# Optimization experiments

Hardware: AMD Instinct MI355X
Metric: run time of the kernel (lower is better)

Reference implementation:

```python
import jax, jax.numpy as jnp
import numpy as np

B, S, E, H, C = 2, 2048, 1024, 16, 16
SQ2 = np.float32(np.sqrt(2.0))


def setup_inputs() -> dict:
    key = jax.random.key(0)
    ks = jax.random.split(key, 32)
    sc = 0.02
    d = {"query": jax.random.normal(ks[0], (B, S, E), jnp.float32)}
    i = 1
    for dom in ("f", "w", "c"):
        d[f"Wp_{dom}"] = jax.random.normal(ks[i], (E, E), jnp.float32) * sc; i += 1
        d[f"bp_{dom}"] = jnp.zeros((E,), jnp.float32)
        d[f"Wc_{dom}"] = jax.random.normal(ks[i], (C, E, 3), jnp.float32) * sc; i += 1
        d[f"bc_{dom}"] = jnp.zeros((C,), jnp.float32)
        d["F" + dom] = jax.random.normal(ks[i], (C, E), jnp.float32); i += 1
    d["mha_iw"] = jax.random.normal(ks[i], (3 * E, E), jnp.float32) * sc; i += 1
    d["mha_ib"] = jnp.zeros((3 * E,), jnp.float32)
    d["mha_ow"] = jax.random.normal(ks[i], (E, E), jnp.float32) * sc; i += 1
    d["mha_ob"] = jnp.zeros((E,), jnp.float32)
    d["fus_W"] = jax.random.normal(ks[i], (E, 3 * E), jnp.float32) * sc; i += 1
    d["fus_b"] = jnp.zeros((E,), jnp.float32)
    return d


def _conv1d(x, W, b):
    # x: [B,S,E] real -> [B,S,C], conv over sequence, kernel 3, same padding
    y = jax.lax.conv_general_dilated(x.transpose(0, 2, 1), W, (1,), [(1, 1)],
                                     dimension_numbers=("NCH", "OIH", "NCH"))
    return (y + b[None, :, None]).transpose(0, 2, 1)


def _channels(x, Wc, bc, Fp):
    # spectral conv (real/imag separately if complex) + adaptive softmax filtering
    if jnp.iscomplexobj(x):
        ch = _conv1d(x.real, Wc, bc) + 1j * _conv1d(x.imag, Wc, bc)
    else:
        ch = _conv1d(x, Wc, bc)
    fw = jax.nn.softmax(Fp, axis=0)  # [C,E], softmax over channels
    return jnp.einsum("bsc,ce->bse", ch, fw.astype(ch.dtype))


def _spec_attn(q, k, v):
    scale = np.float32(1.0) / jnp.sqrt(jnp.asarray(q.shape[-1], jnp.float32))
    scores = jnp.einsum("bse,bte->bst", q, k) * scale
    if jnp.iscomplexobj(scores):
        w = jax.nn.softmax(scores.real, axis=-1)
        cw = (w * jnp.exp(1j * jnp.angle(scores))).astype(jnp.complex64)
        return jnp.einsum("bst,bte->bse", cw, v)
    return jnp.einsum("bst,bte->bse", jax.nn.softmax(scores, axis=-1), v)


def _haar(x):
    # simplified Haar wavelet transform; S is a power of 2 so no padding needed
    cur, coeffs = x, []
    while cur.shape[1] > 1:
        e, o = cur[:, 0::2, :], cur[:, 1::2, :]
        coeffs.append((e - o) / SQ2)
        cur = (e + o) / SQ2
    coeffs.append(cur)
    return jnp.concatenate(coeffs[::-1], axis=1)


def _dct_mats(L):
    n = jnp.arange(L, dtype=jnp.float32)
    k = n[:, None]
    D = jnp.cos(np.pi * k * (2.0 * n + 1.0) / (2.0 * L))
    D = D.at[0].multiply(np.float32(np.sqrt(1.0 / L)))
    D = D.at[1:].multiply(np.float32(np.sqrt(2.0 / L)))
    I = jnp.cos(np.pi * n * (2.0 * k + 1.0) / (2.0 * L))
    I = I.at[:, 0].multiply(np.float32(np.sqrt(1.0 / L)))
    I = I.at[:, 1:].multiply(np.float32(np.sqrt(2.0 / L)))
    return D, I


def _domain(x, Wp, bp, Wc, bc, Fp, domain):
    # key=value=query so q_domain == k_domain == v_domain
    xd = x @ Wp.T + bp
    if domain == "fourier":
        s = jnp.fft.fft(xd, axis=1)
        ch = _channels(s, Wc, bc, Fp)
        out = _spec_attn(ch, ch, ch)
        return jnp.fft.ifft(out, axis=1).real
    elif domain == "wavelet":
        s = _haar(xd)
        ch = _channels(s, Wc, bc, Fp)
        return _spec_attn(ch, ch, ch)  # inverse wavelet is identity in source
    else:  # cosine
        D, I = _dct_mats(xd.shape[1])
        s = jnp.einsum("st,bte->bse", D, xd)
        ch = _channels(s, Wc, bc, Fp)
        out = _spec_attn(ch, ch, ch)
        return jnp.einsum("st,bte->bse", I, out)


def _mha(x, iw, ib, ow, ob, nheads):
    # torch nn.MultiheadAttention (batch_first) self-attention
    Bx, L, Ex = x.shape
    hd = Ex // nheads
    qkv = x @ iw.T + ib
    q, k, v = jnp.split(qkv, 3, axis=-1)
    sh = lambda t: t.reshape(Bx, L, nheads, hd).transpose(0, 2, 1, 3)
    q, k, v = sh(q), sh(k), sh(v)
    a = jax.nn.softmax(jnp.einsum("bhld,bhmd->bhlm", q, k) / np.float32(np.sqrt(hd)), axis=-1)
    o = jnp.einsum("bhlm,bhmd->bhld", a, v).transpose(0, 2, 1, 3).reshape(Bx, L, Ex)
    return o @ ow.T + ob


def reference(query, Wp_f, bp_f, Wc_f, bc_f, Ff, Wp_w, bp_w, Wc_w, bc_w, Fw,
              Wp_c, bp_c, Wc_c, bc_c, Fc, mha_iw, mha_ib, mha_ow, mha_ob, fus_W, fus_b):
    outs = [
        _domain(query, Wp_f, bp_f, Wc_f, bc_f, Ff, "fourier"),
        _domain(query, Wp_w, bp_w, Wc_w, bc_w, Fw, "wavelet"),
        _domain(query, Wp_c, bp_c, Wc_c, bc_c, Fc, "cosine"),
    ]
    Bq, Sq, Eq = query.shape
    stacked = jnp.stack(outs, axis=2)                 # [B,S,3,E]
    corr = _mha(stacked.reshape(Bq * Sq, 3, Eq), mha_iw, mha_ib, mha_ow, mha_ob, H)
    fused = corr.reshape(Bq, Sq, 3 * Eq)              # concat of correlated domain outputs
    return fused @ fus_W.T + fus_b
```

## Files before the change

kernel.cpp:

```cpp
#include <hip/hip_runtime.h>
#include <cmath>

#define BB 2
#define SS_ 2048
#define EE 1024
#define CC 16

typedef __attribute__((ext_vector_type(8))) short short8v;
typedef __attribute__((ext_vector_type(4))) float floatx4;

__device__ __forceinline__ void split4(const float4 v, short4& h, short4& l)
{
    unsigned ux = __float_as_uint(v.x), uy = __float_as_uint(v.y);
    unsigned uz = __float_as_uint(v.z), uw = __float_as_uint(v.w);
    h.x = (short)(ux >> 16); h.y = (short)(uy >> 16);
    h.z = (short)(uz >> 16); h.w = (short)(uw >> 16);
    float lx = v.x - __uint_as_float(ux & 0xFFFF0000u);
    float ly = v.y - __uint_as_float(uy & 0xFFFF0000u);
    float lz = v.z - __uint_as_float(uz & 0xFFFF0000u);
    float lw = v.w - __uint_as_float(uw & 0xFFFF0000u);
    l.x = (short)(__float_as_uint(lx) >> 16);
    l.y = (short)(__float_as_uint(ly) >> 16);
    l.z = (short)(__float_as_uint(lz) >> 16);
    l.w = (short)(__float_as_uint(lw) >> 16);
}

__device__ __forceinline__ void split1(float v, short& h, short& l)
{
    unsigned u = __float_as_uint(v);
    h = (short)(u >> 16);
    float rm = v - __uint_as_float(u & 0xFFFF0000u);
    l = (short)(__float_as_uint(rm) >> 16);
}

__device__ __forceinline__ void split4s(float a, float b, float c, float d,
                                        short4& h, short4& l)
{
    split1(a, h.x, l.x); split1(b, h.y, l.y);
    split1(c, h.z, l.z); split1(d, h.w, l.w);
}

__device__ __forceinline__ void split3_1(float v, short& x1, short& x2, short& x3)
{
    unsigned u = __float_as_uint(v);
    x1 = (short)(u >> 16);
    float r1 = v - __uint_as_float(u & 0xFFFF0000u);
    unsigned u2 = __float_as_uint(r1);
    x2 = (short)(u2 >> 16);
    float r2 = r1 - __uint_as_float(u2 & 0xFFFF0000u);
    x3 = (short)(__float_as_uint(r2) >> 16);
}

__device__ __forceinline__ void split3s(float a, float b, float c, float d,
                                        short4& h1, short4& h2, short4& h3)
{
    split3_1(a, h1.x, h2.x, h3.x); split3_1(b, h1.y, h2.y, h3.y);
    split3_1(c, h1.z, h2.z, h3.z); split3_1(d, h1.w, h2.w, h3.w);
}

__device__ __forceinline__ short4 neg4(short4 a)
{
    short4 r;
    r.x = (short)(a.x ^ (short)0x8000); r.y = (short)(a.y ^ (short)0x8000);
    r.z = (short)(a.z ^ (short)0x8000); r.w = (short)(a.w ^ (short)0x8000);
    return r;
}

__device__ __forceinline__ short8v pack8(short4 a, short4 b)
{
    short8v r;
    r[0] = a.x; r[1] = a.y; r[2] = a.z; r[3] = a.w;
    r[4] = b.x; r[5] = b.y; r[6] = b.z; r[7] = b.w;
    return r;
}

__device__ __forceinline__ short8v negbf(short8v x)
{
    int4 t = *(int4*)&x;
    t.x ^= 0x80008000; t.y ^= 0x80008000;
    t.z ^= 0x80008000; t.w ^= 0x80008000;
    return *(short8v*)&t;
}

#define BM 128
#define BN 128
#define BK 32
#define LDP 40

__launch_bounds__(256, 2)
__global__ void gemm_at(const float* __restrict__ A, const float* __restrict__ Bsrc,
                        float* __restrict__ C,
                        int K, int lda, int ldb, int ldc,
                        long sA, long sB, long sC, float alpha, int KS)
{
    __shared__ short sAh[BM * LDP], sAl[BM * LDP], sBh[BN * LDP], sBl[BN * LDP];
    const int z = blockIdx.z;
    const int bz = z / KS, ks = z % KS;
    const int klen = K / KS, kbase = ks * klen;
    A += (size_t)bz * sA; Bsrc += (size_t)bz * sB; C += (size_t)bz * sC;
    const int tid = threadIdx.x;
    const int m0 = blockIdx.y * BM, n0 = blockIdx.x * BN;

    const int lr0 = tid >> 3;
    const int kc0 = (tid & 7) * 4;
    const float* pa = A + (size_t)(m0 + lr0) * lda + kbase + kc0;
    const float* pb = Bsrc + (size_t)(n0 + lr0) * ldb + kbase + kc0;

    float4 ra[4], rb[4];
    #pragma unroll
    for (int c = 0; c < 4; ++c) {
        ra[c] = *(const float4*)(pa + (size_t)c * 32 * lda);
        rb[c] = *(const float4*)(pb + (size_t)c * 32 * ldb);
    }

    const int lane = tid & 63, wid = tid >> 6;
    const int wm = wid >> 1, wn = wid & 1;
    const int lr = lane & 15, qd = lane >> 4;
    const int arow = wm * 64 + lr;
    const int brow = wn * 64 + lr;
    const int koff = qd * 8;

    floatx4 acc[4][4];
    #pragma unroll
    for (int i = 0; i < 4; ++i)
        #pragma unroll
        for (int j = 0; j < 4; ++j)
            acc[i][j] = (floatx4){0.f, 0.f, 0.f, 0.f};

    for (int kt = 0; kt < klen; kt += BK) {
        __syncthreads();
        #pragma unroll
        for (int c = 0; c < 4; ++c) {
            const int row = lr0 + c * 32;
            short4 h, l;
            split4(ra[c], h, l);
            *(short4*)&sAh[row * LDP + kc0] = h;
            *(short4*)&sAl[row * LDP + kc0] = l;
            split4(rb[c], h, l);
            *(short4*)&sBh[row * LDP + kc0] = h;
            *(short4*)&sBl[row * LDP + kc0] = l;
        }
        __syncthreads();
        if (kt + BK < klen) {
            pa += BK; pb += BK;
            #pragma unroll
            for (int c = 0; c < 4; ++c) {
                ra[c] = *(const float4*)(pa + (size_t)c * 32 * lda);
                rb[c] = *(const float4*)(pb + (size_t)c * 32 * ldb);
            }
        }
        short8v ah[4], al[4], bh[4], bl[4];
        #pragma unroll
        for (int i = 0; i < 4; ++i) {
            ah[i] = *(const short8v*)&sAh[(arow + i * 16) * LDP + koff];
            al[i] = *(const short8v*)&sAl[(arow + i * 16) * LDP + koff];
            bh[i] = *(const short8v*)&sBh[(brow + i * 16) * LDP + koff];
            bl[i] = *(const short8v*)&sBl[(brow + i * 16) * LDP + koff];
        }
        #pragma unroll
        for (int i = 0; i < 4; ++i)
            #pragma unroll
            for (int j = 0; j < 4; ++j)
                acc[i][j] = __builtin_amdgcn_mfma_f32_16x16x32_bf16(ah[i], bh[j], acc[i][j], 0, 0, 0);
        #pragma unroll
        for (int i = 0; i < 4; ++i)
            #pragma unroll
            for (int j = 0; j < 4; ++j)
                acc[i][j] = __builtin_amdgcn_mfma_f32_16x16x32_bf16(ah[i], bl[j], acc[i][j], 0, 0, 0);
        #pragma unroll
        for (int i = 0; i < 4; ++i)
            #pragma unroll
            for (int j = 0; j < 4; ++j)
                acc[i][j] = __builtin_amdgcn_mfma_f32_16x16x32_bf16(al[i], bh[j], acc[i][j], 0, 0, 0);
    }

    #pragma unroll
    for (int i = 0; i < 4; ++i) {
        const int mbase = m0 + wm * 64 + i * 16 + qd * 4;
        #pragma unroll
        for (int j = 0; j < 4; ++j) {
            const int n = n0 + wn * 64 + j * 16 + lr;
            #pragma unroll
            for (int r = 0; r < 4; ++r)
                atomicAdd(&C[(size_t)(mbase + r) * ldc + n], alpha * acc[i][j][r]);
        }
    }
}

template<int NT, int MODE>
__launch_bounds__(256, 4)
__global__ void skmfma(const float* __restrict__ A0, const float* __restrict__ A1,
                       const float* __restrict__ B0, const float* __restrict__ B1,
                       float* __restrict__ C0, float* __restrict__ C1,
                       int K, int lda, int ldb, int ldc,
                       long sA, long sB, long sC, float alpha, int KS)
{
    constexpr int NA = (MODE >= 1) ? 2 : 1;
    constexpr int NB = (MODE == 2) ? 2 : 1;
    constexpr int NACC = (MODE == 1) ? 2 : 1;
    constexpr int CT = NT / 16;
    __shared__ short sAh[NA][64 * 40], sAl[NA][64 * 40];
    __shared__ short sBh[NB][NT * 40], sBl[NB][NT * 40];
    const int z = blockIdx.z;
    const int zb = z / KS, ks = z % KS;
    const int klen = K / KS, kbase = ks * klen;
    const float* Ap[NA]; const float* Bp[NB]; float* Cp[NACC];
    Ap[0] = A0 + (size_t)zb * sA;
    if constexpr (NA == 2) Ap[1] = A1 + (size_t)zb * sA;
    Bp[0] = B0 + (size_t)zb * sB;
    if constexpr (NB == 2) Bp[1] = B1 + (size_t)zb * sB;
    Cp[0] = C0 + (size_t)zb * sC;
    if constexpr (NACC == 2) Cp[1] = C1 + (size_t)zb * sC;

    const int tid = threadIdx.x;
    const int m0 = blockIdx.x * 64;
    const int arow = tid >> 2, akc = (tid & 3) * 8;
    const int lane = tid & 63, w = tid >> 6;
    const int lr = lane & 15, qd = lane >> 4;

    floatx4 acc[NACC][CT];
    #pragma unroll
    for (int s = 0; s < NACC; ++s)
        #pragma unroll
        for (int j = 0; j < CT; ++j)
            acc[s][j] = (floatx4){0.f, 0.f, 0.f, 0.f};

    for (int kc = 0; kc < klen; kc += 32) {
        __syncthreads();
        #pragma unroll
        for (int s = 0; s < NA; ++s) {
            const float* pa = Ap[s] + (size_t)(m0 + arow) * lda + kbase + kc + akc;
            float4 v0 = *(const float4*)pa;
            float4 v1 = *(const float4*)(pa + 4);
            short4 h, l;
            split4(v0, h, l);
            *(short4*)&sAh[s][arow * 40 + akc] = h;
            *(short4*)&sAl[s][arow * 40 + akc] = l;
            split4(v1, h, l);
            *(short4*)&sAh[s][arow * 40 + akc + 4] = h;
            *(short4*)&sAl[s][arow * 40 + akc + 4] = l;
        }
        #pragma unroll
        for (int s = 0; s < NB; ++s) {
            for (int lin = tid; lin < 32 * (NT / 4); lin += 256) {
                int kk = lin / (NT / 4), n4 = (lin % (NT / 4)) * 4;
                float4 v = *(const float4*)(Bp[s] + (size_t)(kbase + kc + kk) * ldb + n4);
                short4 h, l; split4(v, h, l);
                sBh[s][(n4 + 0) * 40 + kk] = h.x; sBh[s][(n4 + 1) * 40 + kk] = h.y;
                sBh[s][(n4 + 2) * 40 + kk] = h.z; sBh[s][(n4 + 3) * 40 + kk] = h.w;
                sBl[s][(n4 + 0) * 40 + kk] = l.x; sBl[s][(n4 + 1) * 40 + kk] = l.y;
                sBl[s][(n4 + 2) * 40 + kk] = l.z; sBl[s][(n4 + 3) * 40 + kk] = l.w;
            }
        }
        __syncthreads();
        short8v ah[NA], alv[NA];
        #pragma unroll
        for (int s = 0; s < NA; ++s) {
            ah[s]  = *(const short8v*)&sAh[s][(w * 16 + lr) * 40 + qd * 8];
            alv[s] = *(const short8v*)&sAl[s][(w * 16 + lr) * 40 + qd * 8];
        }
        short8v bh[NB][CT], bl[NB][CT];
        #pragma unroll
        for (int s = 0; s < NB; ++s)
            #pragma unroll
            for (int j = 0; j < CT; ++j) {
                bh[s][j] = *(const short8v*)&sBh[s][(j * 16 + lr) * 40 + qd * 8];
                bl[s][j] = *(const short8v*)&sBl[s][(j * 16 + lr) * 40 + qd * 8];
            }
        if constexpr (MODE == 0) {
            #pragma unroll
            for (int j = 0; j < CT; ++j) {
                acc[0][j] = __builtin_amdgcn_mfma_f32_16x16x32_bf16(ah[0], bh[0][j], acc[0][j], 0, 0, 0);
                acc[0][j] = __builtin_amdgcn_mfma_f32_16x16x32_bf16(ah[0], bl[0][j], acc[0][j], 0, 0, 0);
                acc[0][j] = __builtin_amdgcn_mfma_f32_16x16x32_bf16(alv[0], bh[0][j], acc[0][j], 0, 0, 0);
            }
        } else if constexpr (MODE == 1) {
            #pragma unroll
            for (int j = 0; j < CT; ++j) {
                acc[0][j] = __builtin_amdgcn_mfma_f32_16x16x32_bf16(ah[0], bh[0][j], acc[0][j], 0, 0, 0);
                acc[0][j] = __builtin_amdgcn_mfma_f32_16x16x32_bf16(ah[0], bl[0][j], acc[0][j], 0, 0, 0);
                acc[0][j] = __builtin_amdgcn_mfma_f32_16x16x32_bf16(alv[0], bh[0][j], acc[0][j], 0, 0, 0);
                acc[1][j] = __builtin_amdgcn_mfma_f32_16x16x32_bf16(ah[1], bh[0][j], acc[1][j], 0, 0, 0);
                acc[1][j] = __builtin_amdgcn_mfma_f32_16x16x32_bf16(ah[1], bl[0][j], acc[1][j], 0, 0, 0);
                acc[1][j] = __builtin_amdgcn_mfma_f32_16x16x32_bf16(alv[1], bh[0][j], acc[1][j], 0, 0, 0);
            }
        } else {
            #pragma unroll
            for (int j = 0; j < CT; ++j) {
                acc[0][j] = __builtin_amdgcn_mfma_f32_16x16x32_bf16(ah[0], bh[0][j], acc[0][j], 0, 0, 0);
                acc[0][j] = __builtin_amdgcn_mfma_f32_16x16x32_bf16(ah[0], bl[0][j], acc[0][j], 0, 0, 0);
                acc[0][j] = __builtin_amdgcn_mfma_f32_16x16x32_bf16(alv[0], bh[0][j], acc[0][j], 0, 0, 0);
                acc[0][j] = __builtin_amdgcn_mfma_f32_16x16x32_bf16(ah[1], bh[1][j], acc[0][j], 0, 0, 0);
                acc[0][j] = __builtin_amdgcn_mfma_f32_16x16x32_bf16(ah[1], bl[1][j], acc[0][j], 0, 0, 0);
                acc[0][j] = __builtin_amdgcn_mfma_f32_16x16x32_bf16(alv[1], bh[1][j], acc[0][j], 0, 0, 0);
            }
        }
    }
    #pragma unroll
    for (int s = 0; s < NACC; ++s)
        #pragma unroll
        for (int j = 0; j < CT; ++j) {
            const int n = j * 16 + lr;
            const int mb = m0 + w * 16 + qd * 4;
            #pragma unroll
            for (int r = 0; r < 4; ++r)
                atomicAdd(&Cp[s][(size_t)(mb + r) * ldc + n], alpha * acc[s][j][r]);
        }
}

__global__ void gen_trig(float* __restrict__ Cc, float* __restrict__ Sn,
                         float* __restrict__ D, float* __restrict__ I)
{
    size_t idx = (size_t)blockIdx.x * 256 + threadIdx.x;
    if (idx < 4194304) {
        int k = (int)(idx >> 11);
        int n = (int)(idx & 2047);
        int m = (k * n) & 2047;
        float ang = (float)(6.283185307179586 * (double)m / 2048.0);
        Cc[idx] = cosf(ang);
        Sn[idx] = -sinf(ang);
    } else {
        idx -= 4194304;
        int i = (int)(idx >> 11);
        int j = (int)(idx & 2047);
        const float r1 = 0.022097086912079608f;
        const float r2 = 0.03125f;
        const float pif = 3.14159265358979323846f;
        float a  = (pif * (float)i) * (float)(2 * j + 1) / 4096.0f;
        D[idx] = cosf(a) * (i == 0 ? r1 : r2);
        float ai = (pif * (float)j) * (float)(2 * i + 1) / 4096.0f;
        I[idx] = cosf(ai) * (j == 0 ? r1 : r2);
    }
}

__launch_bounds__(256)
__global__ void prep_fw_G(const float* __restrict__ F0, const float* __restrict__ F1,
                          const float* __restrict__ F2, float* __restrict__ fwT,
                          float* __restrict__ G)
{
    const int d = blockIdx.x, tid = threadIdx.x;
    const float* Fp = d == 0 ? F0 : (d == 1 ? F1 : F2);
    __shared__ float sf[CC * 1028];
    #pragma unroll
    for (int k = 0; k < 4; ++k) {
        int e = tid + k * 256;
        float v[CC]; float m = -3.4e38f;
        #pragma unroll
        for (int c = 0; c < CC; ++c) { v[c] = Fp[c * EE + e]; m = fmaxf(m, v[c]); }
        float s = 0.f;
        #pragma unroll
        for (int c = 0; c < CC; ++c) { v[c] = expf(v[c] - m); s += v[c]; }
        float inv = 1.f / s;
        #pragma unroll
        for (int c = 0; c < CC; ++c) { v[c] *= inv; sf[c * 1028 + e] = v[c]; }
        #pragma unroll
        for (int j = 0; j < 4; ++j)
            *(float4*)(fwT + d * 16384 + (size_t)e * 16 + j * 4) = *(float4*)&v[j * 4];
    }
    __syncthreads();
    const int a = tid >> 4, b = tid & 15;
    const float4* pa = (const float4*)&sf[a * 1028];
    const float4* pb = (const float4*)&sf[b * 1028];
    float s = 0.f;
    for (int i = 0; i < 256; ++i) {
        float4 x = pa[i], y = pb[i];
        s += x.x * y.x + x.y * y.y + x.z * y.z + x.w * y.w;
    }
    G[d * 256 + a * 16 + b] = s * 0.03125f;
}

__global__ void build_w2(const float* __restrict__ W0, const float* __restrict__ W1,
                         const float* __restrict__ W2_, float* __restrict__ W2cat)
{
    int idx = blockIdx.x * 256 + threadIdx.x;
    if (idx >= 3 * CC * EE * 3) return;
    int d = idx / 49152, r = idx % 49152;
    const float* Wc = d == 0 ? W0 : (d == 1 ? W1 : W2_);
    int c = r / 3072, e = (r % 3072) / 3, k = r % 3;
    W2cat[d * 49152 + e * 48 + c * 3 + k] = Wc[r];
}

__global__ void build_ub2(const float* __restrict__ b0, const float* __restrict__ b1,
                          const float* __restrict__ b2, const float* __restrict__ W2cat,
                          float* __restrict__ ub)
{
    const int d = blockIdx.x, tid = threadIdx.x;
    const float* bp = d == 0 ? b0 : (d == 1 ? b1 : b2);
    __shared__ float red[4][48];
    const int c = tid & 63, sl = tid >> 6;
    float s = 0.f;
    if (c < 48)
        for (int e = sl; e < EE; e += 4)
            s += bp[e] * W2cat[d * 49152 + e * 48 + c];
    if (c < 48) red[sl][c] = s;
    __syncthreads();
    if (tid < 48) ub[d * 48 + tid] = red[0][tid] + red[1][tid] + red[2][tid] + red[3][tid];
}

__launch_bounds__(256)
__global__ void build_yb2(const float* __restrict__ ob, const float* __restrict__ fus_W,
                          const float* __restrict__ fus_b, float* __restrict__ yb)
{
    const int n = blockIdx.x * 4 + (threadIdx.x >> 6);
    const int lane = threadIdx.x & 63;
    float s = 0.f;
    for (int j = lane; j < 3072; j += 64)
        s += ob[j & 1023] * fus_W[(size_t)n * 3072 + j];
    #pragma unroll
    for (int off = 32; off > 0; off >>= 1) s += __shfl_xor(s, off, 64);
    if (lane == 0) yb[n] = s + fus_b[n];
}

__global__ void init_all(float* __restrict__ zone1, const float* __restrict__ ub,
                         float* __restrict__ Pt, float* __restrict__ FTb,
                         float* __restrict__ out, const float* __restrict__ yb)
{
    size_t idx = (size_t)blockIdx.x * 256 + threadIdx.x;
    const size_t W3N = 147456, UN = 589824, ZN = 720896;
    const size_t Z1 = W3N + UN + ZN;
    const size_t PTN = 156672, FTN = 3145728, ON = 4194304;
    if (idx < Z1) {
        float v = 0.f;
        if (idx >= W3N && idx < W3N + UN) {
            size_t r = idx - W3N;
            int d = (int)(r / 196608), c = (int)(r % 48);
            v = ub[d * 48 + c];
        }
        zone1[idx] = v;
    } else if (idx < Z1 + PTN) {
        Pt[idx - Z1] = 0.f;
    } else if (idx < Z1 + PTN + FTN) {
        FTb[idx - Z1 - PTN] = 0.f;
    } else if (idx < Z1 + PTN + FTN + ON) {
        size_t r = idx - Z1 - PTN - FTN;
        out[r] = yb[r & 1023];
    }
}

__global__ void ib_append(const float* __restrict__ ib, float* __restrict__ Pt)
{
    int idx = blockIdx.x * 256 + threadIdx.x;
    if (idx >= 9216) return;
    int d = idx / 3072, j = idx % 3072;
    Pt[d * 52224 + j * 17 + 16] = ib[j];
}

__launch_bounds__(256)
__global__ void build_M(const float* __restrict__ Pt, float* __restrict__ Mten)
{
    int blk = blockIdx.x;
    int h = blk / 9, lm = blk % 9;
    int l = lm / 3, m = lm % 3;
    __shared__ float sQ[64][17], sK[64][17];
    for (int lin = threadIdx.x; lin < 1088; lin += 256) {
        int d = lin / 17, a = lin % 17;
        sQ[d][a] = Pt[l * 52224 + (size_t)(h * 64 + d) * 17 + a];
        sK[d][a] = Pt[m * 52224 + (size_t)(1024 + h * 64 + d) * 17 + a];
    }
    __syncthreads();
    for (int o = threadIdx.x; o < 289; o += 256) {
        int a = o / 17, b = o % 17;
        float s = 0.f;
        for (int d = 0; d < 64; ++d) s += sQ[d][a] * sK[d][b];
        Mten[(size_t)blk * 289 + o] = 0.125f * s;
    }
}

__global__ void transpose_k(const float* __restrict__ X, float* __restrict__ XT,
                            int rows, int cols)
{
    __shared__ float tile[32][33];
    const int lx = threadIdx.x & 31, ly = threadIdx.x >> 5;
    const int r0 = blockIdx.y * 32, c0 = blockIdx.x * 32;
    #pragma unroll
    for (int p = 0; p < 4; ++p)
        tile[ly + p * 8][lx] = X[(size_t)(r0 + ly + p * 8) * cols + c0 + lx];
    __syncthreads();
    #pragma unroll
    for (int p = 0; p < 4; ++p)
        XT[(size_t)(c0 + ly + p * 8) * rows + r0 + lx] = tile[lx][ly + p * 8];
}

__global__ void transpose_wp3(const float* __restrict__ W0, const float* __restrict__ W1,
                              const float* __restrict__ W2, float* __restrict__ WT)
{
    __shared__ float tile[32][33];
    const float* X = blockIdx.z == 0 ? W0 : (blockIdx.z == 1 ? W1 : W2);
    float* T = WT + (size_t)blockIdx.z * 1048576;
    const int lx = threadIdx.x & 31, ly = threadIdx.x >> 5;
// ... 172 lines not shown
    split3s(ki.x, ki.y, ki.z, ki.w, s1, s2, s3);
    *(short4*)&AqF[row * 96 + jj * 4]      = q1;
    *(short4*)&AqF[row * 96 + 16 + jj * 4] = p1;
    *(short4*)&AqF[row * 96 + 32 + jj * 4] = q2;
    *(short4*)&AqF[row * 96 + 48 + jj * 4] = p2;
    *(short4*)&AqF[row * 96 + 64 + jj * 4] = q3;
    *(short4*)&AqF[row * 96 + 80 + jj * 4] = p3;
    *(short4*)&BreF[row * 96 + jj * 4]      = r1;
    *(short4*)&BreF[row * 96 + 16 + jj * 4] = neg4(s1);
    *(short4*)&BreF[row * 96 + 32 + jj * 4] = r2;
    *(short4*)&BreF[row * 96 + 48 + jj * 4] = neg4(s2);
    *(short4*)&BreF[row * 96 + 64 + jj * 4] = r3;
    *(short4*)&BreF[row * 96 + 80 + jj * 4] = neg4(s3);
    *(short4*)&BimF[row * 96 + jj * 4]      = s1;
    *(short4*)&BimF[row * 96 + 16 + jj * 4] = r1;
    *(short4*)&BimF[row * 96 + 32 + jj * 4] = s2;
    *(short4*)&BimF[row * 96 + 48 + jj * 4] = r2;
    *(short4*)&BimF[row * 96 + 64 + jj * 4] = s3;
    *(short4*)&BimF[row * 96 + 80 + jj * 4] = r3;
    {
        float v0 = chFr[vsrc], v1 = chFr[vsrc + 16];
        float v2 = chFr[vsrc + 32], v3 = chFr[vsrc + 48];
        short4 h, l; split4s(v0, v1, v2, v3, h, l);
        *(short4*)&VtFrH[vo] = h;
        *(short4*)&VtFrL[vo] = l;
        v0 = chFi[vsrc]; v1 = chFi[vsrc + 16];
        v2 = chFi[vsrc + 32]; v3 = chFi[vsrc + 48];
        split4s(v0, v1, v2, v3, h, l);
        *(short4*)&VtFiH[vo] = h;
        *(short4*)&VtFiL[vo] = l;
    }
}


__launch_bounds__(256)
__global__ void flash_stats(const short* __restrict__ AqF, const short* __restrict__ BreF,
                            const short* __restrict__ AqW, const short* __restrict__ KsW,
                            const short* __restrict__ AqC, const short* __restrict__ KsC,
                            float* __restrict__ Mpart, float* __restrict__ Lpart)
{
    const int z = blockIdx.z, dom = z >> 1, b = z & 1;
    const int tid = threadIdx.x, w = tid >> 6, lane = tid & 63;
    const int lr = lane & 15, qd = lane >> 4;
    const int rowbase = blockIdx.x * 64 + w * 16;
    const int ks = blockIdx.y;
    const size_t qrow = (size_t)b * 2048 + rowbase + lr;
    const floatx4 FZ = {0.f, 0.f, 0.f, 0.f};
    float m[4] = {-3.4e38f, -3.4e38f, -3.4e38f, -3.4e38f};
    float l[4] = {0.f, 0.f, 0.f, 0.f};
    if (dom == 0) {
        const short8v a1 = *(const short8v*)&AqF[qrow * 96 + qd * 8];
        const short8v a2 = *(const short8v*)&AqF[qrow * 96 + 32 + qd * 8];
        const short8v a3 = *(const short8v*)&AqF[qrow * 96 + 64 + qd * 8];
        const short* Bb = BreF + (size_t)b * 2048 * 96;
        for (int s = 0; s < 32; ++s) {
            const short* brow = Bb + (size_t)(ks * 512 + s * 16 + lr) * 96;
            short8v b1 = *(const short8v*)&brow[qd * 8];
            short8v b2 = *(const short8v*)&brow[32 + qd * 8];
            short8v b3 = *(const short8v*)&brow[64 + qd * 8];
            floatx4 sc = __builtin_amdgcn_mfma_f32_16x16x32_bf16(a1, b1, FZ, 0, 0, 0);
            sc = __builtin_amdgcn_mfma_f32_16x16x32_bf16(a1, b2, sc, 0, 0, 0);
            sc = __builtin_amdgcn_mfma_f32_16x16x32_bf16(a2, b1, sc, 0, 0, 0);
            sc = __builtin_amdgcn_mfma_f32_16x16x32_bf16(a1, b3, sc, 0, 0, 0);
            sc = __builtin_amdgcn_mfma_f32_16x16x32_bf16(a2, b2, sc, 0, 0, 0);
            sc = __builtin_amdgcn_mfma_f32_16x16x32_bf16(a3, b1, sc, 0, 0, 0);
            #pragma unroll
            for (int r = 0; r < 4; ++r) {
                float v = sc[r];
                if (v <= m[r]) l[r] += __expf(v - m[r]);
                else { l[r] = l[r] * __expf(m[r] - v) + 1.f; m[r] = v; }
            }
        }
    } else {
        const short* Aq = dom == 1 ? AqW : AqC;
        const short* Ks = dom == 1 ? KsW : KsC;
        const short8v a1 = *(const short8v*)&Aq[qrow * 48 + qd * 8];
        const short8v a2 = *(const short8v*)&Aq[qrow * 48 + 32 + (qd & 1) * 8];
        const short* Kb = Ks + (size_t)b * 2048 * 48;
        const int ko = (qd & 1) * 8;
        for (int s = 0; s < 32; ++s) {
            const short* krow = Kb + (size_t)(ks * 512 + s * 16 + lr) * 48;
            short8v b1  = *(const short8v*)&krow[ko];
            short8v b2  = *(const short8v*)&krow[16 + ko];
            short8v b3  = *(const short8v*)&krow[32 + ko];
            short8v b12 = *(const short8v*)&krow[qd * 8];
            floatx4 sc = __builtin_amdgcn_mfma_f32_16x16x32_bf16(a1, b1, FZ, 0, 0, 0);
            sc = __builtin_amdgcn_mfma_f32_16x16x32_bf16(a1, b2, sc, 0, 0, 0);
            sc = __builtin_amdgcn_mfma_f32_16x16x32_bf16(a1, b3, sc, 0, 0, 0);
            sc = __builtin_amdgcn_mfma_f32_16x16x32_bf16(a2, b12, sc, 0, 0, 0);
            #pragma unroll
            for (int r = 0; r < 4; ++r) {
                float v = sc[r];
                if (v <= m[r]) l[r] += __expf(v - m[r]);
                else { l[r] = l[r] * __expf(m[r] - v) + 1.f; m[r] = v; }
            }
        }
    }
    #pragma unroll
    for (int off = 1; off < 16; off <<= 1) {
        #pragma unroll
        for (int r = 0; r < 4; ++r) {
            float m2 = __shfl_xor(m[r], off, 64);
            float l2 = __shfl_xor(l[r], off, 64);
            float mn = fmaxf(m[r], m2);
            l[r] = l[r] * __expf(m[r] - mn) + l2 * __expf(m2 - mn);
            m[r] = mn;
        }
    }
    if (lr == 0) {
        size_t base = ((size_t)z * 4 + ks) * 2048 + rowbase + qd * 4;
        #pragma unroll
        for (int r = 0; r < 4; ++r) { Mpart[base + r] = m[r]; Lpart[base + r] = l[r]; }
    }
}

__global__ void flash_merge(const float* __restrict__ Mpart, const float* __restrict__ Lpart,
                            float* __restrict__ Mrow, float* __restrict__ Linv,
                            float* __restrict__ Ozone)
{
    size_t idx = (size_t)blockIdx.x * 256 + threadIdx.x;
    if (idx < 12288) {
        size_t s = idx >> 11, r = idx & 2047;
        float m = -3.4e38f;
        #pragma unroll
        for (int k = 0; k < 4; ++k) m = fmaxf(m, Mpart[(s * 4 + k) * 2048 + r]);
        float l = 0.f;
        #pragma unroll
        for (int k = 0; k < 4; ++k)
            l += Lpart[(s * 4 + k) * 2048 + r] * __expf(Mpart[(s * 4 + k) * 2048 + r] - m);
        Mrow[idx] = m;
        Linv[idx] = 1.f / l;
    } else if (idx < 12288 + 262144) {
        Ozone[idx - 12288] = 0.f;
    }
}

__launch_bounds__(256)
__global__ void flash_pv(const short* __restrict__ AqF, const short* __restrict__ BreF,
                         const short* __restrict__ BimF,
                         const short* __restrict__ VtFrH, const short* __restrict__ VtFrL,
                         const short* __restrict__ VtFiH, const short* __restrict__ VtFiL,
                         const short* __restrict__ AqW, const short* __restrict__ KsW,
                         const short* __restrict__ VtWH, const short* __restrict__ VtWL,
                         const short* __restrict__ AqC, const short* __restrict__ KsC,
                         const short* __restrict__ VtCH, const short* __restrict__ VtCL,
                         const float* __restrict__ Mrow, const float* __restrict__ Linv,
                         float* __restrict__ OFr, float* __restrict__ OFi,
                         float* __restrict__ Ow_, float* __restrict__ Oc_)
{
    __shared__ float sP[4][1152];
    const int z = blockIdx.z, dom = z >> 1, b = z & 1;
    const int tid = threadIdx.x, w = tid >> 6, lane = tid & 63;
    const int lr = lane & 15, qd = lane >> 4;
    const int rowbase = blockIdx.x * 64 + w * 16;
    const int ks = blockIdx.y;
    const size_t qrow = (size_t)b * 2048 + rowbase + lr;
    const floatx4 FZ = {0.f, 0.f, 0.f, 0.f};
    float* P0 = &sP[w][0];
    const float4 m4 = *(const float4*)&Mrow[(size_t)z * 2048 + rowbase + qd * 4];
    const float4 li4 = *(const float4*)&Linv[(size_t)z * 2048 + rowbase + qd * 4];
    const float mA[4] = {m4.x, m4.y, m4.z, m4.w};
    const float liA[4] = {li4.x, li4.y, li4.z, li4.w};

    if (dom != 0) {
        const short* Aq = dom == 1 ? AqW : AqC;
        const short* Ks = dom == 1 ? KsW : KsC;
        const short* VH = dom == 1 ? VtWH : VtCH;
        const short* VL = dom == 1 ? VtWL : VtCL;
        float* O = dom == 1 ? Ow_ : Oc_;
        const short8v a1 = *(const short8v*)&Aq[qrow * 48 + qd * 8];
        const short8v a2 = *(const short8v*)&Aq[qrow * 48 + 32 + (qd & 1) * 8];
        const short* Kb = Ks + (size_t)b * 2048 * 48;
        const short* vhB = VH + (size_t)(b * 16 + lr) * 2048;
        const short* vlB = VL + (size_t)(b * 16 + lr) * 2048;
        const int ko = (qd & 1) * 8;
        floatx4 acc = FZ;
        for (int c = 0; c < 16; ++c) {
            const int tt = ks * 512 + c * 32;
            #pragma unroll
            for (int s2 = 0; s2 < 2; ++s2) {
                const short* krow = Kb + (size_t)(tt + s2 * 16 + lr) * 48;
                short8v b1  = *(const short8v*)&krow[ko];
                short8v b2  = *(const short8v*)&krow[16 + ko];
                short8v b3  = *(const short8v*)&krow[32 + ko];
                short8v b12 = *(const short8v*)&krow[qd * 8];
                floatx4 sc = __builtin_amdgcn_mfma_f32_16x16x32_bf16(a1, b1, FZ, 0, 0, 0);
                sc = __builtin_amdgcn_mfma_f32_16x16x32_bf16(a1, b2, sc, 0, 0, 0);
                sc = __builtin_amdgcn_mfma_f32_16x16x32_bf16(a1, b3, sc, 0, 0, 0);
                sc = __builtin_amdgcn_mfma_f32_16x16x32_bf16(a2, b12, sc, 0, 0, 0);
                #pragma unroll
                for (int r = 0; r < 4; ++r)
                    P0[(qd * 4 + r) * 36 + s2 * 16 + lr] = __expf(sc[r] - mA[r]);
            }
            asm volatile("s_waitcnt lgkmcnt(0)" ::: "memory");
            __builtin_amdgcn_sched_barrier(0);
            float4 p0 = *(const float4*)&P0[lr * 36 + qd * 8];
            float4 p1 = *(const float4*)&P0[lr * 36 + qd * 8 + 4];
            short4 h0, g0, h1, g1;
            split4s(p0.x, p0.y, p0.z, p0.w, h0, g0);
            split4s(p1.x, p1.y, p1.z, p1.w, h1, g1);
            short8v ph = pack8(h0, h1), pl = pack8(g0, g1);
            short8v vh = *(const short8v*)&vhB[tt + qd * 8];
            short8v vl = *(const short8v*)&vlB[tt + qd * 8];
            acc = __builtin_amdgcn_mfma_f32_16x16x32_bf16(ph, vh, acc, 0, 0, 0);
            acc = __builtin_amdgcn_mfma_f32_16x16x32_bf16(ph, vl, acc, 0, 0, 0);
            acc = __builtin_amdgcn_mfma_f32_16x16x32_bf16(pl, vh, acc, 0, 0, 0);
        }
        size_t ob = ((size_t)b * 2048 + rowbase + qd * 4) * 16 + lr;
        #pragma unroll
        for (int r = 0; r < 4; ++r)
            atomicAdd(&O[ob + (size_t)r * 16], acc[r] * liA[r]);
        return;
    }
    const short8v a1 = *(const short8v*)&AqF[qrow * 96 + qd * 8];
    const short8v a2 = *(const short8v*)&AqF[qrow * 96 + 32 + qd * 8];
    const short8v a3 = *(const short8v*)&AqF[qrow * 96 + 64 + qd * 8];
    const short* BrB = BreF + (size_t)b * 2048 * 96;
    const short* BiB = BimF + (size_t)b * 2048 * 96;
    const short* vrhB = VtFrH + (size_t)(b * 16 + lr) * 2048;
    const short* vrlB = VtFrL + (size_t)(b * 16 + lr) * 2048;
    const short* vihB = VtFiH + (size_t)(b * 16 + lr) * 2048;
    const short* vilB = VtFiL + (size_t)(b * 16 + lr) * 2048;
    float* PR = P0;
    float* PI = P0 + 576;
    floatx4 accR = FZ, accI = FZ;
    for (int c = 0; c < 16; ++c) {
        const int tt = ks * 512 + c * 32;
        #pragma unroll
        for (int s2 = 0; s2 < 2; ++s2) {
            const short* br = BrB + (size_t)(tt + s2 * 16 + lr) * 96;
            const short* bi = BiB + (size_t)(tt + s2 * 16 + lr) * 96;
            short8v b1r = *(const short8v*)&br[qd * 8];
            short8v b2r = *(const short8v*)&br[32 + qd * 8];
            short8v b3r = *(const short8v*)&br[64 + qd * 8];
            short8v b1i = *(const short8v*)&bi[qd * 8];
            short8v b2i = *(const short8v*)&bi[32 + qd * 8];
            short8v b3i = *(const short8v*)&bi[64 + qd * 8];
            floatx4 sre = __builtin_amdgcn_mfma_f32_16x16x32_bf16(a1, b1r, FZ, 0, 0, 0);
            sre = __builtin_amdgcn_mfma_f32_16x16x32_bf16(a1, b2r, sre, 0, 0, 0);
            sre = __builtin_amdgcn_mfma_f32_16x16x32_bf16(a2, b1r, sre, 0, 0, 0);
            sre = __builtin_amdgcn_mfma_f32_16x16x32_bf16(a1, b3r, sre, 0, 0, 0);
            sre = __builtin_amdgcn_mfma_f32_16x16x32_bf16(a2, b2r, sre, 0, 0, 0);
            sre = __builtin_amdgcn_mfma_f32_16x16x32_bf16(a3, b1r, sre, 0, 0, 0);
            floatx4 sim = __builtin_amdgcn_mfma_f32_16x16x32_bf16(a1, b1i, FZ, 0, 0, 0);
            sim = __builtin_amdgcn_mfma_f32_16x16x32_bf16(a1, b2i, sim, 0, 0, 0);
            sim = __builtin_amdgcn_mfma_f32_16x16x32_bf16(a2, b1i, sim, 0, 0, 0);
            sim = __builtin_amdgcn_mfma_f32_16x16x32_bf16(a1, b3i, sim, 0, 0, 0);
            sim = __builtin_amdgcn_mfma_f32_16x16x32_bf16(a2, b2i, sim, 0, 0, 0);
            sim = __builtin_amdgcn_mfma_f32_16x16x32_bf16(a3, b1i, sim, 0, 0, 0);
            #pragma unroll
            for (int r = 0; r < 4; ++r) {
                float xr = sre[r], xi = sim[r];
                float p = __expf(xr - mA[r]);
                float rr = sqrtf(xr * xr + xi * xi);
                float t = p / rr;
                float wr = (rr > 0.f) ? xr * t : p;
                float wi = (rr > 0.f) ? xi * t : 0.f;
                PR[(qd * 4 + r) * 36 + s2 * 16 + lr] = wr;
                PI[(qd * 4 + r) * 36 + s2 * 16 + lr] = wi;
            }
        }
        asm volatile("s_waitcnt lgkmcnt(0)" ::: "memory");
        __builtin_amdgcn_sched_barrier(0);
        float4 r0 = *(const float4*)&PR[lr * 36 + qd * 8];
        float4 r1 = *(const float4*)&PR[lr * 36 + qd * 8 + 4];
        float4 i0 = *(const float4*)&PI[lr * 36 + qd * 8];
        float4 i1 = *(const float4*)&PI[lr * 36 + qd * 8 + 4];
        short4 ha, la, hb, lb;
        split4s(r0.x, r0.y, r0.z, r0.w, ha, la);
        split4s(r1.x, r1.y, r1.z, r1.w, hb, lb);
        short8v wrh = pack8(ha, hb), wrl = pack8(la, lb);
        split4s(i0.x, i0.y, i0.z, i0.w, ha, la);
        split4s(i1.x, i1.y, i1.z, i1.w, hb, lb);
        short8v wih = pack8(ha, hb), wil = pack8(la, lb);
        short8v wihN = negbf(wih), wilN = negbf(wil);
        short8v vrh = *(const short8v*)&vrhB[tt + qd * 8];
        short8v vrl = *(const short8v*)&vrlB[tt + qd * 8];
        short8v vih = *(const short8v*)&vihB[tt + qd * 8];
        short8v vil = *(const short8v*)&vilB[tt + qd * 8];
        accR = __builtin_amdgcn_mfma_f32_16x16x32_bf16(wrh, vrh, accR, 0, 0, 0);
        accR = __builtin_amdgcn_mfma_f32_16x16x32_bf16(wrh, vrl, accR, 0, 0, 0);
        accR = __builtin_amdgcn_mfma_f32_16x16x32_bf16(wrl, vrh, accR, 0, 0, 0);
        accR = __builtin_amdgcn_mfma_f32_16x16x32_bf16(wihN, vih, accR, 0, 0, 0);
        accR = __builtin_amdgcn_mfma_f32_16x16x32_bf16(wihN, vil, accR, 0, 0, 0);
        accR = __builtin_amdgcn_mfma_f32_16x16x32_bf16(wilN, vih, accR, 0, 0, 0);
        accI = __builtin_amdgcn_mfma_f32_16x16x32_bf16(wrh, vih, accI, 0, 0, 0);
        accI = __builtin_amdgcn_mfma_f32_16x16x32_bf16(wrh, vil, accI, 0, 0, 0);
        accI = __builtin_amdgcn_mfma_f32_16x16x32_bf16(wrl, vih, accI, 0, 0, 0);
        accI = __builtin_amdgcn_mfma_f32_16x16x32_bf16(wih, vrh, accI, 0, 0, 0);
        accI = __builtin_amdgcn_mfma_f32_16x16x32_bf16(wih, vrl, accI, 0, 0, 0);
        accI = __builtin_amdgcn_mfma_f32_16x16x32_bf16(wil, vrh, accI, 0, 0, 0);
    }
    size_t ob = ((size_t)b * 2048 + rowbase + qd * 4) * 16 + lr;
    #pragma unroll
    for (int r = 0; r < 4; ++r) {
        atomicAdd(&OFr[ob + (size_t)r * 16], accR[r] * liA[r]);
        atomicAdd(&OFi[ob + (size_t)r * 16], accI[r] * liA[r]);
    }
}

__launch_bounds__(256)
__global__ void mha_o(const float* __restrict__ R0, const float* __restrict__ R1,
                      const float* __restrict__ R2, const float* __restrict__ Pt,
                      const float* __restrict__ Mten, float* __restrict__ MO)
{
    const int tid = threadIdx.x;
    const int p = blockIdx.x * 256 + tid;
    const int h = blockIdx.y;
    __shared__ float sPv[3 * 64 * 20];
    __shared__ float sM[9 * 17 * 20];
    for (int lin = tid; lin < 3264; lin += 256) {
        int mm = lin / 1088, rem = lin % 1088;
        int rr = rem / 17, a = rem % 17;
        sPv[(mm * 64 + rr) * 20 + a] = Pt[mm * 52224 + (size_t)(2048 + h * 64 + rr) * 17 + a];
    }
    for (int lin = tid; lin < 2601; lin += 256) {
        int lm = lin / 289, rem = lin % 289;
        int a = rem / 17, bq = rem % 17;
        sM[lm * 340 + a * 20 + bq] = Mten[(size_t)h * 2601 + lin];
    }
    __syncthreads();
    float R[3][16];
    float4 R4[3][4];
    #pragma unroll
    for (int j = 0; j < 4; ++j) {
        R4[0][j] = *(const float4*)(R0 + (size_t)p * 16 + j * 4);
        R4[1][j] = *(const float4*)(R1 + (size_t)p * 16 + j * 4);
        R4[2][j] = *(const float4*)(R2 + (size_t)p * 16 + j * 4);
        *(float4*)&R[0][j * 4] = R4[0][j];
        *(float4*)&R[1][j * 4] = R4[1][j];
        *(float4*)&R[2][j * 4] = R4[2][j];
    }
    float w[3][3];
    #pragma unroll
    for (int l = 0; l < 3; ++l) {
        float sc[3];
        #pragma unroll
        for (int mm = 0; mm < 3; ++mm) {
            const float* Mp = &sM[(l * 3 + mm) * 340];
            float s = 0.f;
            #pragma unroll
            for (int a = 0; a < 17; ++a) {
                const float* mr = Mp + a * 20;
                float4 m0 = *(const float4*)(mr), m1 = *(const float4*)(mr + 4);
                float4 m2 = *(const float4*)(mr + 8), m3 = *(const float4*)(mr + 12);
                float t = mr[16];
                t = fmaf(m0.x, R4[mm][0].x, t); t = fmaf(m0.y, R4[mm][0].y, t);
                t = fmaf(m0.z, R4[mm][0].z, t); t = fmaf(m0.w, R4[mm][0].w, t);
                t = fmaf(m1.x, R4[mm][1].x, t); t = fmaf(m1.y, R4[mm][1].y, t);
                t = fmaf(m1.z, R4[mm][1].z, t); t = fmaf(m1.w, R4[mm][1].w, t);
                t = fmaf(m2.x, R4[mm][2].x, t); t = fmaf(m2.y, R4[mm][2].y, t);
                t = fmaf(m2.z, R4[mm][2].z, t); t = fmaf(m2.w, R4[mm][2].w, t);
                t = fmaf(m3.x, R4[mm][3].x, t); t = fmaf(m3.y, R4[mm][3].y, t);
                t = fmaf(m3.z, R4[mm][3].z, t); t = fmaf(m3.w, R4[mm][3].w, t);
                float ra = (a < 16) ? R[l][a] : 1.f;
                s = fmaf(ra, t, s);
            }
            sc[mm] = s;
        }
        float mx = fmaxf(sc[0], fmaxf(sc[1], sc[2]));
        float e0 = expf(sc[0] - mx), e1 = expf(sc[1] - mx), e2 = expf(sc[2] - mx);
        float inv = 1.f / (e0 + e1 + e2);
        w[l][0] = e0 * inv; w[l][1] = e1 * inv; w[l][2] = e2 * inv;
    }
    #pragma unroll
    for (int d4 = 0; d4 < 16; ++d4) {
        float4 vm[3];
        #pragma unroll
        for (int mm = 0; mm < 3; ++mm) {
            float vx[4];
            #pragma unroll
            for (int r = 0; r < 4; ++r) {
                const float* pv = &sPv[(mm * 64 + d4 * 4 + r) * 20];
                float4 p0 = *(const float4*)(pv), p1 = *(const float4*)(pv + 4);
                float4 p2 = *(const float4*)(pv + 8), p3 = *(const float4*)(pv + 12);
                float t = pv[16];
                t = fmaf(R4[mm][0].x, p0.x, t); t = fmaf(R4[mm][0].y, p0.y, t);
                t = fmaf(R4[mm][0].z, p0.z, t); t = fmaf(R4[mm][0].w, p0.w, t);
                t = fmaf(R4[mm][1].x, p1.x, t); t = fmaf(R4[mm][1].y, p1.y, t);
                t = fmaf(R4[mm][1].z, p1.z, t); t = fmaf(R4[mm][1].w, p1.w, t);
                t = fmaf(R4[mm][2].x, p2.x, t); t = fmaf(R4[mm][2].y, p2.y, t);
                t = fmaf(R4[mm][2].z, p2.z, t); t = fmaf(R4[mm][2].w, p2.w, t);
                t = fmaf(R4[mm][3].x, p3.x, t); t = fmaf(R4[mm][3].y, p3.y, t);
                t = fmaf(R4[mm][3].w, p3.w, t); t = fmaf(R4[mm][3].z, p3.z, t);
                vx[r] = t;
            }
            vm[mm] = (float4){vx[0], vx[1], vx[2], vx[3]};
        }
        #pragma unroll
        for (int l = 0; l < 3; ++l) {
            float4 o4;
            o4.x = w[l][0] * vm[0].x + w[l][1] * vm[1].x + w[l][2] * vm[2].x;
            o4.y = w[l][0] * vm[0].y + w[l][1] * vm[1].y + w[l][2] * vm[2].y;
            o4.z = w[l][0] * vm[0].z + w[l][1] * vm[1].z + w[l][2] * vm[2].z;
            o4.w = w[l][0] * vm[0].w + w[l][1] * vm[1].w + w[l][2] * vm[2].w;
            *(float4*)(MO + (size_t)p * 3072 + l * 1024 + h * 64 + d4 * 4) = o4;
        }
    }
}

extern "C" void kernel_launch(void* const* d_in, const int* in_sizes, int n_in,
                              void* d_out, int out_size, void* d_ws, size_t ws_size,
                              hipStream_t stream)
{
    const float* query = (const float*)d_in[0];
    const float* Wp[3] = {(const float*)d_in[1], (const float*)d_in[6],  (const float*)d_in[11]};
    const float* bp[3] = {(const float*)d_in[2], (const float*)d_in[7],  (const float*)d_in[12]};
    const float* Wc[3] = {(const float*)d_in[3], (const float*)d_in[8],  (const float*)d_in[13]};
    const float* bc[3] = {(const float*)d_in[4], (const float*)d_in[9],  (const float*)d_in[14]};
    const float* Fp[3] = {(const float*)d_in[5], (const float*)d_in[10], (const float*)d_in[15]};
    const float* mha_iw = (const float*)d_in[16];
    const float* mha_ib = (const float*)d_in[17];
    const float* mha_ow = (const float*)d_in[18];
    const float* mha_ob = (const float*)d_in[19];
    const float* fus_W  = (const float*)d_in[20];
    const float* fus_b  = (const float*)d_in[21];
    float* out = (float*)d_out;
    float* ws = (float*)d_ws;

    size_t off = 0;
    auto alloc = [&](size_t n) { float* p = ws + off; off += n; return p; };
    float* MAT0 = alloc(4194304);
    float* MAT1 = alloc(4194304);
    float* DCTD = alloc(4194304);
    float* DCTI = alloc(4194304);
    float* MO   = alloc((size_t)4096 * 3072);
    float* FTb  = alloc((size_t)1024 * 3072);
    float* OWT  = alloc((size_t)1024 * 1024);
    float* WpT  = alloc(3145728);
    float* fwT  = alloc(49152);
    float* W2cat = alloc(147456);
    float* ubv  = alloc(256);
    float* Gm   = alloc(1024);
    float* W3cat = alloc(147456);
    float* Ucat = alloc(589824);
    float* Tfr  = alloc(196608);
    float* Tfi  = alloc(196608);
    float* Tc   = alloc(196608);
    float* Rf   = alloc(65536);
    float* Rc   = alloc(65536);
    float* Tw   = alloc(196608);
    float* chFr = alloc(65536); float* chFi = alloc(65536);
    float* QpFr = alloc(65536); float* QpFi = alloc(65536);
    float* chW  = alloc(65536); float* QpW  = alloc(65536);
    float* chC  = alloc(65536); float* QpC  = alloc(65536);
    float* OFr  = alloc(65536); float* OFi  = alloc(65536);
    float* Ow   = alloc(65536); float* Oc   = alloc(65536);
    float* Pt   = alloc(156672);
    float* Mten = alloc(41616);
    float* ybv  = alloc(1024);
    if (ws_size < off * sizeof(float)) return;

    size_t poff = 0;
    auto palloc = [&](size_t n) { float* p = WpT + poff; poff += n; return p; };
    float* AqW  = palloc(98304);
    float* KsW  = palloc(98304);
    float* AqC  = palloc(98304);
    float* KsC  = palloc(98304);
    float* VtWH = palloc(32768); float* VtWL = palloc(32768);
    float* VtCH = palloc(32768); float* VtCL = palloc(32768);
    float* AqF  = palloc(196608);
    float* BreF = palloc(196608);
    float* BimF = palloc(196608);
    float* VtFrH = palloc(32768); float* VtFrL = palloc(32768);
    float* VtFiH = palloc(32768); float* VtFiL = palloc(32768);
    float* Mpart = palloc(49152); float* Lpart = palloc(49152);
    float* MrowA = palloc(12288); float* LinvA = palloc(12288);

    float* Uf = Ucat, *Uw = Ucat + 196608, *Uc = Ucat + 2 * 196608;
    const long SE48 = 2048 * 48, SE16 = 2048 * 16;

    build_w2<<<dim3(576), dim3(256), 0, stream>>>(Wc[0], Wc[1], Wc[2], W2cat);
    prep_fw_G<<<dim3(3), dim3(256), 0, stream>>>(Fp[0], Fp[1], Fp[2], fwT, Gm);
    build_ub2<<<dim3(3), dim3(256), 0, stream>>>(bp[0], bp[1], bp[2], W2cat, ubv);
    build_yb2<<<dim3(256), dim3(256), 0, stream>>>(mha_ob, fus_W, fus_b, ybv);
    gen_trig<<<dim3(32768), dim3(256), 0, stream>>>(MAT0, MAT1, DCTD, DCTI);
    transpose_wp3<<<dim3(32, 32, 3), dim3(256), 0, stream>>>(Wp[0], Wp[1], Wp[2], WpT);
    init_all<<<dim3(34980), dim3(256), 0, stream>>>(W3cat, ubv, Pt, FTb, out, ybv);

    skmfma<48, 0><<<dim3(16, 1, 6), dim3(256), 0, stream>>>(
        WpT, nullptr, W2cat, nullptr, W3cat, nullptr,
        1024, 1024, 48, 48, 1048576, 49152, 49152, 1.f, 2);
    skmfma<48, 0><<<dim3(64, 1, 6), dim3(256), 0, stream>>>(
        query, nullptr, W3cat, nullptr, Ucat, nullptr,
        1024, 1024, 48, 48, 0, 49152, 196608, 1.f, 2);
    skmfma<48, 1><<<dim3(32, 1, 8), dim3(256), 0, stream>>>(
        MAT0, MAT1, Uf, nullptr, Tfr, Tfi,
        2048, 2048, 48, 48, 0, SE48, SE48, 1.f, 4);
    skmfma<48, 0><<<dim3(32, 1, 8), dim3(256), 0, stream>>>(
        DCTD, nullptr, Uc, nullptr, Tc, nullptr,
        2048, 2048, 48, 48, 0, SE48, SE48, 1.f, 4);

    haar_all<<<dim3(12, 2), dim3(256), 0, stream>>>(Uw, Tw);

    conv_all<<<dim3(32, 2, 3), dim3(256), 0, stream>>>(
        Tfr, Tfi, Tw, Tc, Gm, bc[0], bc[1], bc[2],
        chFr, chFi, chW, chC, QpFr, QpFi, QpW, QpC);

    prep_flash<<<dim3(32, 2, 3), dim3(256), 0, stream>>>(
        QpFr, QpFi, chFr, chFi, QpW, chW, QpC, chC,
        (short*)AqF, (short*)BreF, (short*)BimF,
        (short*)VtFrH, (short*)VtFrL, (short*)VtFiH, (short*)VtFiL,
        (short*)AqW, (short*)KsW, (short*)VtWH, (short*)VtWL,
        (short*)AqC, (short*)KsC, (short*)VtCH, (short*)VtCL);
    flash_stats<<<dim3(32, 4, 6), dim3(256), 0, stream>>>(
        (const short*)AqF, (const short*)BreF,
        (const short*)AqW, (const short*)KsW,
        (const short*)AqC, (const short*)KsC, Mpart, Lpart);
    flash_merge<<<dim3(1072), dim3(256), 0, stream>>>(Mpart, Lpart, MrowA, LinvA, OFr);
    flash_pv<<<dim3(32, 4, 6), dim3(256), 0, stream>>>(
        (const short*)AqF, (const short*)BreF, (const short*)BimF,
        (const short*)VtFrH, (const short*)VtFrL, (const short*)VtFiH, (const short*)VtFiL,
        (const short*)AqW, (const short*)KsW, (const short*)VtWH, (const short*)VtWL,
        (const short*)AqC, (const short*)KsC, (const short*)VtCH, (const short*)VtCL,
        MrowA, LinvA, OFr, OFi, Ow, Oc);

    skmfma<16, 2><<<dim3(32, 1, 8), dim3(256), 0, stream>>>(
        MAT0, MAT1, OFr, OFi, Rf, nullptr,
        2048, 2048, 16, 16, 0, SE16, SE16, 1.f / 2048.f, 4);
    skmfma<16, 0><<<dim3(32, 1, 8), dim3(256), 0, stream>>>(
        DCTI, nullptr, Oc, nullptr, Rc, nullptr,
        2048, 2048, 16, 16, 0, SE16, SE16, 1.f, 4);
    skmfma<16, 0><<<dim3(48, 1, 6), dim3(256), 0, stream>>>(
        mha_iw, nullptr, fwT, nullptr, Pt, nullptr,
        1024, 1024, 16, 17, 0, 16384, 52224, 1.f, 2);

    ib_append<<<dim3(36), dim3(256), 0, stream>>>(mha_ib, Pt);
    build_M<<<dim3(144), dim3(256), 0, stream>>>(Pt, Mten);

    mha_o<<<dim3(16, 16), dim3(256), 0, stream>>>(Rf, Ow, Rc, Pt, Mten, MO);

    transpose_k<<<dim3(32, 32), dim3(256), 0, stream>>>(mha_ow, OWT, 1024, 1024);
    gemm_at<<<dim3(8, 8, 12), dim3(256), 0, stream>>>(
        fus_W, OWT, FTb, 1024, 3072, 1024, 3072, 1024, 0, 1024, 1.f, 4);

    gemm_at<<<dim3(8, 32, 4), dim3(256), 0, stream>>>(
        MO, FTb, out, 3072, 3072, 3072, 1024, 0, 0, 0, 1.f, 4);
}
```

Measured before the change: 754.0 us.

## Emit pre-split bf16 hi/lo operands from mha_o and use pre-split final GEMM

mha_o now writes its output as bf16 high/low halves instead of fp32, FTb is split into hi/lo by a new kernel, and the final fusion GEMM uses a new gemm_bt kernel that loads pre-split bf16 operands directly. This removes repeated in-loop fp32 splitting and halves the bytes moved per operand element in the big final GEMM. Split-K for both GEMMs is also reduced, cutting atomic traffic. The split buffers reuse the MO and DCTD workspace regions, which relies on those regions being large enough and not otherwise live.

```diff
diff --git a/kernel.cpp b/kernel.cpp
--- a/kernel.cpp
+++ b/kernel.cpp
@@ -185,6 +185,118 @@
                 atomicAdd(&C[(size_t)(mbase + r) * ldc + n], alpha * acc[i][j][r]);
         }
     }
+}
+
+__launch_bounds__(256, 2)
+__global__ void gemm_bt(const short* __restrict__ Ah, const short* __restrict__ Al,
+                        const short* __restrict__ Bh, const short* __restrict__ Bl,
+                        float* __restrict__ C,
+                        int K, int lda, int ldb, int ldc, float alpha, int KS)
+{
+    __shared__ short sAh[BM * LDP], sAl[BM * LDP], sBh[BN * LDP], sBl[BN * LDP];
+    const int ks = blockIdx.z % KS;
+    const int klen = K / KS, kbase = ks * klen;
+    const int tid = threadIdx.x;
+    const int m0 = blockIdx.y * BM, n0 = blockIdx.x * BN;
+
+    const int lr0 = tid >> 3;
+    const int kc0 = (tid & 7) * 4;
+    const short* pah = Ah + (size_t)(m0 + lr0) * lda + kbase + kc0;
+    const short* pal = Al + (size_t)(m0 + lr0) * lda + kbase + kc0;
+    const short* pbh = Bh + (size_t)(n0 + lr0) * ldb + kbase + kc0;
+    const short* pbl = Bl + (size_t)(n0 + lr0) * ldb + kbase + kc0;
+
+    short4 rah[4], ral[4], rbh[4], rbl[4];
+    #pragma unroll
+    for (int c = 0; c < 4; ++c) {
+        rah[c] = *(const short4*)(pah + (size_t)c * 32 * lda);
+        ral[c] = *(const short4*)(pal + (size_t)c * 32 * lda);
+        rbh[c] = *(const short4*)(pbh + (size_t)c * 32 * ldb);
+        rbl[c] = *(const short4*)(pbl + (size_t)c * 32 * ldb);
+    }
+
+    const int lane = tid & 63, wid = tid >> 6;
+    const int wm = wid >> 1, wn = wid & 1;
+    const int lr = lane & 15, qd = lane >> 4;
+    const int arow = wm * 64 + lr;
+    const int brow = wn * 64 + lr;
+    const int koff = qd * 8;
+
+    floatx4 acc[4][4];
+    #pragma unroll
+    for (int i = 0; i < 4; ++i)
+        #pragma unroll
+        for (int j = 0; j < 4; ++j)
+            acc[i][j] = (floatx4){0.f, 0.f, 0.f, 0.f};
+
+    for (int kt = 0; kt < klen; kt += BK) {
+        __syncthreads();
+        #pragma unroll
+        for (int c = 0; c < 4; ++c) {
+            const int row = lr0 + c * 32;
+            *(short4*)&sAh[row * LDP + kc0] = rah[c];
+            *(short4*)&sAl[row * LDP + kc0] = ral[c];
+            *(short4*)&sBh[row * LDP + kc0] = rbh[c];
+            *(short4*)&sBl[row * LDP + kc0] = rbl[c];
+        }
+        __syncthreads();
+        if (kt + BK < klen) {
+            pah += BK; pal += BK; pbh += BK; pbl += BK;
+            #pragma unroll
+            for (int c = 0; c < 4; ++c) {
+                rah[c] = *(const short4*)(pah + (size_t)c * 32 * lda);
+                ral[c] = *(const short4*)(pal + (size_t)c * 32 * lda);
+                rbh[c] = *(const short4*)(pbh + (size_t)c * 32 * ldb);
+                rbl[c] = *(const short4*)(pbl + (size_t)c * 32 * ldb);
+            }
+        }
+        short8v ah[4], al[4], bh[4], bl[4];
+        #pragma unroll
+        for (int i = 0; i < 4; ++i) {
+            ah[i] = *(const short8v*)&sAh[(arow + i * 16) * LDP + koff];
+            al[i] = *(const short8v*)&sAl[(arow + i * 16) * LDP + koff];
+            bh[i] = *(const short8v*)&sBh[(brow + i * 16) * LDP + koff];
+            bl[i] = *(const short8v*)&sBl[(brow + i * 16) * LDP + koff];
+        }
+        #pragma unroll
+        for (int i = 0; i < 4; ++i)
+            #pragma unroll
+            for (int j = 0; j < 4; ++j)
+                acc[i][j] = __builtin_amdgcn_mfma_f32_16x16x32_bf16(ah[i], bh[j], acc[i][j], 0, 0, 0);
+        #pragma unroll
+        for (int i = 0; i < 4; ++i)
+            #pragma unroll
+            for (int j = 0; j < 4; ++j)
+                acc[i][j] = __builtin_amdgcn_mfma_f32_16x16x32_bf16(ah[i], bl[j], acc[i][j], 0, 0, 0);
+        #pragma unroll
+        for (int i = 0; i < 4; ++i)
+            #pragma unroll
+            for (int j = 0; j < 4; ++j)
+                acc[i][j] = __builtin_amdgcn_mfma_f32_16x16x32_bf16(al[i], bh[j], acc[i][j], 0, 0, 0);
+    }
+
+    #pragma unroll
+    for (int i = 0; i < 4; ++i) {
+        const int mbase = m0 + wm * 64 + i * 16 + qd * 4;
+        #pragma unroll
+        for (int j = 0; j < 4; ++j) {
+            const int n = n0 + wn * 64 + j * 16 + lr;
+            #pragma unroll
+            for (int r = 0; r < 4; ++r)
+                atomicAdd(&C[(size_t)(mbase + r) * ldc + n], alpha * acc[i][j][r]);
+        }
+    }
+}
+
+__global__ void ftb_split(const float* __restrict__ X, short* __restrict__ Xh,
+                          short* __restrict__ Xl, int n4)
+{
+    int idx = blockIdx.x * 256 + threadIdx.x;
+    if (idx >= n4) return;
+    float4 v = *(const float4*)(X + (size_t)idx * 4);
+    short4 h, l; split4(v, h, l);
+    *(short4*)&Xh[(size_t)idx * 4] = h;
+    *(short4*)&Xl[(size_t)idx * 4] = l;
 }
 
 template<int NT, int MODE>
@@ -963,7 +1075,8 @@
 __launch_bounds__(256)
 __global__ void mha_o(const float* __restrict__ R0, const float* __restrict__ R1,
                       const float* __restrict__ R2, const float* __restrict__ Pt,
-                      const float* __restrict__ Mten, float* __restrict__ MO)
+                      const float* __restrict__ Mten,
+                      short* __restrict__ MOh, short* __restrict__ MOl)
 {
     const int tid = threadIdx.x;
     const int p = blockIdx.x * 256 + tid;
@@ -1055,7 +1168,11 @@
             o4.y = w[l][0] * vm[0].y + w[l][1] * vm[1].y + w[l][2] * vm[2].y;
             o4.z = w[l][0] * vm[0].z + w[l][1] * vm[1].z + w[l][2] * vm[2].z;
             o4.w = w[l][0] * vm[0].w + w[l][1] * vm[1].w + w[l][2] * vm[2].w;
-            *(float4*)(MO + (size_t)p * 3072 + l * 1024 + h * 64 + d4 * 4) = o4;
+            short4 hh, ll;
+            split4s(o4.x, o4.y, o4.z, o4.w, hh, ll);
+            size_t oidx = (size_t)p * 3072 + l * 1024 + h * 64 + d4 * 4;
+            *(short4*)&MOh[oidx] = hh;
+            *(short4*)&MOl[oidx] = ll;
         }
     }
 }
@@ -1128,6 +1245,11 @@
     float* Mpart = palloc(49152); float* Lpart = palloc(49152);
     float* MrowA = palloc(12288); float* LinvA = palloc(12288);
 
+    short* MOh = (short*)MO;
+    short* MOl = MOh + (size_t)4096 * 3072;
+    short* FTbh = (short*)DCTD;
+    short* FTbl = FTbh + (size_t)1024 * 3072;
+
     float* Uf = Ucat, *Uw = Ucat + 196608, *Uc = Ucat + 2 * 196608;
     const long SE48 = 2048 * 48, SE16 = 2048 * 16;
 
@@ -1189,12 +1311,14 @@
     ib_append<<<dim3(36), dim3(256), 0, stream>>>(mha_ib, Pt);
     build_M<<<dim3(144), dim3(256), 0, stream>>>(Pt, Mten);
 
-    mha_o<<<dim3(16, 16), dim3(256), 0, stream>>>(Rf, Ow, Rc, Pt, Mten, MO);
+    mha_o<<<dim3(16, 16), dim3(256), 0, stream>>>(Rf, Ow, Rc, Pt, Mten, MOh, MOl);
 
     transpose_k<<<dim3(32, 32), dim3(256), 0, stream>>>(mha_ow, OWT, 1024, 1024);
-    gemm_at<<<dim3(8, 8, 12), dim3(256), 0, stream>>>(
-        fus_W, OWT, FTb, 1024, 3072, 1024, 3072, 1024, 0, 1024, 1.f, 4);
-
-    gemm_at<<<dim3(8, 32, 4), dim3(256), 0, stream>>>(
-        MO, FTb, out, 3072, 3072, 3072, 1024, 0, 0, 0, 1.f, 4);
-}
+    gemm_at<<<dim3(8, 8, 6), dim3(256), 0, stream>>>(
+        fus_W, OWT, FTb, 1024, 3072, 1024, 3072, 1024, 0, 1024, 1.f, 2);
+
+    ftb_split<<<dim3(3072), dim3(256), 0, stream>>>(FTb, FTbh, FTbl, 786432);
+
+    gemm_bt<<<dim3(8, 32, 2), dim3(256), 0, stream>>>(
+        MOh, MOl, FTbh, FTbl, out, 3072, 3072, 3072, 1024, 1.f, 2);
+}
```

Result: faster. 734.6 us (-2.6%).
